# Kernel tuning notes

Hardware: AMD Instinct MI355X
Metric: run time of the kernel (lower is better)

The kernel has to match this reference:

```python
import jax, jax.numpy as jnp
import numpy as np

N_BITS = 6
N_STATES = 1 << N_BITS  # 64
BATCH = 262144
SINKHORN_ITERS = 50
EPS = 0.1
TINY = 1e-8


def hamming_cost(n_bits: int) -> jnp.ndarray:
    """(2^n, 2^n) Hamming distance between all binary states (== torch.cdist p=0)."""
    n = 1 << n_bits
    states = (np.arange(n)[:, None] >> np.arange(n_bits)[None, :]) & 1  # (n, n_bits)
    dist = (states[:, None, :] != states[None, :, :]).sum(-1)           # (n, n)
    return jnp.asarray(dist, dtype=jnp.float32)


def setup_inputs() -> dict:
    key = jax.random.key(0)
    k1, k2 = jax.random.split(key)
    p = jax.random.uniform(k1, (BATCH, N_STATES), dtype=jnp.float32)
    q = jax.random.uniform(k2, (BATCH, N_STATES), dtype=jnp.float32)
    cost_matrix = hamming_cost(N_BITS)  # registered buffer in the torch module
    return {"p": p, "q": q, "cost_matrix": cost_matrix}


def reference(p, q, cost_matrix):
    # normalize with the same epsilon smoothing as the torch module
    p = p + TINY
    q = q + TINY
    p = p / p.sum(axis=-1, keepdims=True)
    q = q / q.sum(axis=-1, keepdims=True)

    K = jnp.exp(-cost_matrix / EPS)  # (n, n)

    def step(carry, _):
        u, _v = carry
        # torch: (K.T @ u[...,None]).squeeze(-1)  ==  u @ K
        v = q / (u @ K)
        # torch: (K @ v[...,None]).squeeze(-1)    ==  v @ K.T
        u_new = p / (v @ K.T)
        return (u_new, v), None

    init = (jnp.ones_like(p), jnp.ones_like(q))
    (u, v), _ = jax.lax.scan(step, init, None, length=SINKHORN_ITERS)

    # emd_b = sum_ij u_bi * K_ij * v_bj * C_ij, without materializing (B,n,n)
    emd = jnp.einsum("bi,ij,bj->b", u, K * cost_matrix, v)
    return emd
```

## Files before the change

### kernel.cpp

```cpp
#include <hip/hip_runtime.h>


namespace {

constexpr int   N     = 64;
constexpr int   NBITS = 6;
constexpr int   ITERS = 50;
constexpr float TINY  = 1e-8f;

constexpr double Ad = 4.5399929762484854e-05;
constexpr float  A  = (float)Ad;
constexpr double ROWSUM6 = (1.0 + Ad) * (1.0 + Ad) * (1.0 + Ad) *
                           (1.0 + Ad) * (1.0 + Ad) * (1.0 + Ad);
constexpr float  C0 = (float)(1.0 / ROWSUM6);
constexpr float  EMD_SCALE = (float)(Ad / (1.0 - Ad * Ad));
constexpr float  EMD_DIAG  = (float)(6.0 * Ad * Ad / (1.0 - Ad * Ad));

__device__ __forceinline__ float rcp(float x) { return __builtin_amdgcn_rcpf(x); }

__device__ __forceinline__ void butterfly(float w[N]) {
#pragma unroll
  for (int b = 0; b < NBITS; ++b) {
#pragma unroll
    for (int i = 0; i < N; ++i) {
      if ((i & (1 << b)) == 0) {
        const int j = i | (1 << b);
        const float wi = w[i];
        const float wj = w[j];
        w[i] = fmaf(A, wj, wi);
        w[j] = fmaf(A, wi, wj);
      }
    }
  }
}

__global__ __launch_bounds__(256, 2) void emd_sinkhorn_kernel(
    const float* __restrict__ gp, const float* __restrict__ gq,
    float* __restrict__ out, int nbatch) {
  const int b = blockIdx.x * 256 + threadIdx.x;
  if (b >= nbatch) return;

  float p[N], q[N], w[N];

  const float4* __restrict__ p4 =
      reinterpret_cast<const float4*>(gp) + (size_t)b * (N / 4);
  const float4* __restrict__ q4 =
      reinterpret_cast<const float4*>(gq) + (size_t)b * (N / 4);

  float ps = 0.f, qs = 0.f;
#pragma unroll
  for (int k = 0; k < N / 4; ++k) {
    const float4 tp = p4[k];
    p[4 * k + 0] = tp.x + TINY;
    p[4 * k + 1] = tp.y + TINY;
    p[4 * k + 2] = tp.z + TINY;
    p[4 * k + 3] = tp.w + TINY;
    const float4 tq = q4[k];
    q[4 * k + 0] = tq.x + TINY;
    q[4 * k + 1] = tq.y + TINY;
    q[4 * k + 2] = tq.z + TINY;
    q[4 * k + 3] = tq.w + TINY;
  }
#pragma unroll
  for (int i = 0; i < N; ++i) { ps += p[i]; qs += q[i]; }
  const float rp = rcp(ps);
  const float rq = rcp(qs);
#pragma unroll
  for (int i = 0; i < N; ++i) { p[i] *= rp; q[i] *= rq; }

#pragma unroll
  for (int i = 0; i < N; ++i) w[i] = q[i] * C0;

#pragma unroll 1
  for (int it = 0; it < ITERS - 1; ++it) {
    butterfly(w);
#pragma unroll
    for (int i = 0; i < N; ++i) w[i] = p[i] * rcp(w[i]);
    butterfly(w);
#pragma unroll
    for (int i = 0; i < N; ++i) w[i] = q[i] * rcp(w[i]);
  }

  butterfly(w);

  float s0 = 0.f;
  float sx = 0.f;
#pragma unroll
  for (int i = 0; i < N; ++i) {
    const float ui = p[i] * rcp(w[i]);
    s0 = fmaf(ui, w[i], s0);
#pragma unroll
    for (int bb = 0; bb < NBITS; ++bb) {
      sx = fmaf(ui, w[i ^ (1 << bb)], sx);
    }
  }

  out[b] = sx * EMD_SCALE - s0 * EMD_DIAG;
}

}

extern "C" void kernel_launch(void* const* d_in, const int* in_sizes, int n_in,
                              void* d_out, int out_size, void* d_ws, size_t ws_size,
                              hipStream_t stream) {
  const float* p = (const float*)d_in[0];
  const float* q = (const float*)d_in[1];
  float* out = (float*)d_out;

  const int nbatch = in_sizes[0] / N;
  const int block = 256;
  const int grid = (nbatch + block - 1) / block;
  emd_sinkhorn_kernel<<<grid, block, 0, stream>>>(p, q, out, nbatch);
}
```

Before: 482.2 us.

## Drop p/q register arrays, reload inputs per iteration, raise occupancy

Removes the 128 registers per thread that held normalized p and q. Instead the kernel re-reads the raw float4 inputs from global memory inside every Sinkhorn half-step, and launch bounds go from 2 to 4 blocks per SIMD. It also uses Sinkhorn's scale invariance to skip the normalization and the TINY offset, dividing the final sum by the p total once at the end. The cost is heavy repeated global traffic: the per-thread input working set across active waves is far larger than L1/L2, so each iteration may stream from HBM. It also introduces a small numerical deviation from dropping TINY.

```diff
diff --git a/kernel.cpp b/kernel.cpp
--- a/kernel.cpp
+++ b/kernel.cpp
@@ -6,13 +6,9 @@
 constexpr int   N     = 64;
 constexpr int   NBITS = 6;
 constexpr int   ITERS = 50;
-constexpr float TINY  = 1e-8f;
 
 constexpr double Ad = 4.5399929762484854e-05;
 constexpr float  A  = (float)Ad;
-constexpr double ROWSUM6 = (1.0 + Ad) * (1.0 + Ad) * (1.0 + Ad) *
-                           (1.0 + Ad) * (1.0 + Ad) * (1.0 + Ad);
-constexpr float  C0 = (float)(1.0 / ROWSUM6);
 constexpr float  EMD_SCALE = (float)(Ad / (1.0 - Ad * Ad));
 constexpr float  EMD_DIAG  = (float)(6.0 * Ad * Ad / (1.0 - Ad * Ad));
 
@@ -34,68 +30,71 @@
   }
 }
 
-__global__ __launch_bounds__(256, 2) void emd_sinkhorn_kernel(
+__global__ __launch_bounds__(256, 4) void emd_sinkhorn_kernel(
     const float* __restrict__ gp, const float* __restrict__ gq,
     float* __restrict__ out, int nbatch) {
   const int b = blockIdx.x * 256 + threadIdx.x;
   if (b >= nbatch) return;
-
-  float p[N], q[N], w[N];
 
   const float4* __restrict__ p4 =
       reinterpret_cast<const float4*>(gp) + (size_t)b * (N / 4);
   const float4* __restrict__ q4 =
       reinterpret_cast<const float4*>(gq) + (size_t)b * (N / 4);
 
-  float ps = 0.f, qs = 0.f;
+  float w[N];
+
 #pragma unroll
   for (int k = 0; k < N / 4; ++k) {
-    const float4 tp = p4[k];
-    p[4 * k + 0] = tp.x + TINY;
-    p[4 * k + 1] = tp.y + TINY;
-    p[4 * k + 2] = tp.z + TINY;
-    p[4 * k + 3] = tp.w + TINY;
-    const float4 tq = q4[k];
-    q[4 * k + 0] = tq.x + TINY;
-    q[4 * k + 1] = tq.y + TINY;
-    q[4 * k + 2] = tq.z + TINY;
-    q[4 * k + 3] = tq.w + TINY;
+    const float4 t = q4[k];
+    w[4 * k + 0] = t.x;
+    w[4 * k + 1] = t.y;
+    w[4 * k + 2] = t.z;
+    w[4 * k + 3] = t.w;
   }
-#pragma unroll
-  for (int i = 0; i < N; ++i) { ps += p[i]; qs += q[i]; }
-  const float rp = rcp(ps);
-  const float rq = rcp(qs);
-#pragma unroll
-  for (int i = 0; i < N; ++i) { p[i] *= rp; q[i] *= rq; }
-
-#pragma unroll
-  for (int i = 0; i < N; ++i) w[i] = q[i] * C0;
 
 #pragma unroll 1
   for (int it = 0; it < ITERS - 1; ++it) {
     butterfly(w);
 #pragma unroll
-    for (int i = 0; i < N; ++i) w[i] = p[i] * rcp(w[i]);
+    for (int k = 0; k < N / 4; ++k) {
+      const float4 t = p4[k];
+      w[4 * k + 0] = t.x * rcp(w[4 * k + 0]);
+      w[4 * k + 1] = t.y * rcp(w[4 * k + 1]);
+      w[4 * k + 2] = t.z * rcp(w[4 * k + 2]);
+      w[4 * k + 3] = t.w * rcp(w[4 * k + 3]);
+    }
     butterfly(w);
 #pragma unroll
-    for (int i = 0; i < N; ++i) w[i] = q[i] * rcp(w[i]);
+    for (int k = 0; k < N / 4; ++k) {
+      const float4 t = q4[k];
+      w[4 * k + 0] = t.x * rcp(w[4 * k + 0]);
+      w[4 * k + 1] = t.y * rcp(w[4 * k + 1]);
+      w[4 * k + 2] = t.z * rcp(w[4 * k + 2]);
+      w[4 * k + 3] = t.w * rcp(w[4 * k + 3]);
+    }
   }
 
   butterfly(w);
 
-  float s0 = 0.f;
+  float sp = 0.f;
   float sx = 0.f;
 #pragma unroll
-  for (int i = 0; i < N; ++i) {
-    const float ui = p[i] * rcp(w[i]);
-    s0 = fmaf(ui, w[i], s0);
+  for (int k = 0; k < N / 4; ++k) {
+    const float4 t = p4[k];
+    const float pv[4] = {t.x, t.y, t.z, t.w};
 #pragma unroll
-    for (int bb = 0; bb < NBITS; ++bb) {
-      sx = fmaf(ui, w[i ^ (1 << bb)], sx);
+    for (int j = 0; j < 4; ++j) {
+      const int i = 4 * k + j;
+      sp += pv[j];
+      const float ui = pv[j] * rcp(w[i]);
+      float nb = w[i ^ 1];
+#pragma unroll
+      for (int bb = 1; bb < NBITS; ++bb) nb += w[i ^ (1 << bb)];
+      sx = fmaf(ui, nb, sx);
     }
   }
 
-  out[b] = sx * EMD_SCALE - s0 * EMD_DIAG;
+  out[b] = fmaf(sx * rcp(sp), EMD_SCALE, -EMD_DIAG);
 }
 
 }
```

New measurement: 820.1 us. 70.1% more time.
